# Kernel optimization log

Measured on AMD Instinct MI355X. Metric: run time of the kernel, lower is better.

## Reference

```python
import jax, jax.numpy as jnp
import numpy as np

J = 21        # joints per skeleton
DIM = 3       # cfg.dataset.dim
NH = 7        # node_hsize = 2*DIM + 1
H = 4         # cfg.model.gat_heads
HD = 64       # h_dim
ALPHA = 0.2   # cfg.model.gat_alpha (LeakyReLU slope)


def setup_inputs() -> dict:
    key = jax.random.key(0)
    k1, k2, k3, k4, k5 = jax.random.split(key, 5)
    inputs = jax.random.normal(k1, (16, 1024, J * NH), dtype=jnp.float32)
    starts = jnp.arange(8, dtype=jnp.int64) * 128
    seq_start_end = jnp.stack([starts, starts + 128], axis=1)  # [8,2], unused in forward
    # Xavier-ish scaled params
    W_heads = jax.random.normal(k2, (H, NH, HD), dtype=jnp.float32) * (1.414 / np.sqrt(NH + HD) * np.sqrt(6) / 1.732)
    a_heads = jax.random.normal(k3, (H, 2 * HD), dtype=jnp.float32) * 0.1
    W_out = jax.random.normal(k4, (H * HD, HD), dtype=jnp.float32) * 0.08
    a_out = jax.random.normal(k5, (2 * HD,), dtype=jnp.float32) * 0.1
    return {"inputs": inputs, "seq_start_end": seq_start_end,
            "W_heads": W_heads, "a_heads": a_heads,
            "W_out": W_out, "a_out": a_out}


def _gat_attend(h, a1, a2):
    # h: [..., J, D]; a1,a2: [..., D] broadcastable; FC graph -> no adj mask
    f1 = jnp.sum(h * a1[..., None, :], axis=-1)          # [..., J]
    f2 = jnp.sum(h * a2[..., None, :], axis=-1)          # [..., J]
    e = jax.nn.leaky_relu(f1[..., :, None] + f2[..., None, :], ALPHA)  # [..., J, J]
    attn = jax.nn.softmax(e, axis=-1)
    return jnp.matmul(attn, h)                           # [..., J, D]


def reference(inputs, seq_start_end, W_heads, a_heads, W_out, a_out):
    F_, P, _ = inputs.shape
    # rebuild per-node graph features: [offset(dim) | loc(dim) | S(1)] per joint
    off = inputs[..., : J * DIM].reshape(F_, P, J, DIM)
    loc = inputs[..., J * DIM: 2 * J * DIM].reshape(F_, P, J, DIM)
    S = inputs[..., 2 * J * DIM:].reshape(F_, P, J, 1)
    x = jnp.concatenate([off, loc, S], axis=-1)          # [F,P,J,NH]
    # multi-head GAT layer (concat=True -> elu)
    h = jnp.einsum('fpjn,hnd->fphjd', x, W_heads)        # [F,P,H,J,HD]
    a1 = a_heads[:, :HD]                                 # [H,HD]
    a2 = a_heads[:, HD:]
    hp = jax.nn.elu(_gat_attend(h, a1[None, None], a2[None, None]))  # [F,P,H,J,HD]
    xcat = jnp.transpose(hp, (0, 1, 3, 2, 4)).reshape(F_, P, J, H * HD)
    # output GAT layer (concat=False -> raw h_prime), then outer elu + log_softmax
    h2 = jnp.einsum('fpjn,nd->fpjd', xcat, W_out)        # [F,P,J,HD]
    hp2 = _gat_attend(h2, a_out[None, None, :HD], a_out[None, None, HD:])
    out = jax.nn.log_softmax(jax.nn.elu(hp2), axis=-1)   # log_softmax over feature dim
    return out.reshape(F_, P, J * HD)
```

## Files before the change

kernel.cpp:

```cpp
#include <hip/hip_runtime.h>
#include <hip/hip_bf16.h>
#include <math.h>

#define J   21
#define NH  7
#define H   4
#define HD  64
#define ALPHA 0.2f

#define HPS  264
#define JPA  40
#define JPT  24
#define F12S 24
#define ROW2 68

#define LDS_FLOATS 6612

typedef __attribute__((ext_vector_type(8))) short short8;
typedef __attribute__((ext_vector_type(4))) float floatx4;

static __device__ __forceinline__ short f2bf(float f) {
    __hip_bfloat16 h = __float2bfloat16(f);
    return __builtin_bit_cast(short, h);
}
static __device__ __forceinline__ short hi16(float f) {
    return (short)(__builtin_bit_cast(unsigned, f) >> 16);
}
static __device__ __forceinline__ unsigned pack2hi(float lo, float hi) {
    return __builtin_amdgcn_perm(__builtin_bit_cast(unsigned, hi),
                                 __builtin_bit_cast(unsigned, lo), 0x07060302u);
}
static __device__ __forceinline__ float elu(float a) {
    return (a > 0.f) ? a : (__expf(a) - 1.f);
}

__global__ void preconv(const float* __restrict__ Wo, const float* __restrict__ Wh,
                        const float* __restrict__ ah, short* __restrict__ ws) {
    int t = blockIdx.x * 256 + threadIdx.x;
    if (t < 16384) {
        int n = t >> 8, k = t & 255;
        ws[t] = f2bf(Wo[k * HD + n]);
    } else if (t < 18432) {
        int i = t - 16384;
        int hh = i >> 9, d = (i >> 3) & 63, n = i & 7;
        ws[t] = (n < 7) ? f2bf(Wh[(hh * NH + n) * HD + d]) : (short)0;
    } else if (t < 18496) {
        int i = t - 18432;
        int hh = i >> 4, s = (i >> 3) & 1, n = i & 7;
        float acc = 0.f;
        if (n < 7) {
            for (int d = 0; d < HD; d++)
                acc += Wh[(hh * NH + n) * HD + d] * ah[hh * 2 * HD + s * HD + d];
        }
        ((float*)(ws + 18432))[i] = acc;
    }
}

__global__ __launch_bounds__(256, 6)
void gat_kernel(const float* __restrict__ inp,
                const float* __restrict__ ao,
                const short* __restrict__ ws,
                float* __restrict__ out)
{
    __shared__ __align__(16) float smem[LDS_FLOATS];
    short* hp_bf  = (short*)smem;
    float* f1o    = smem;
    float* f2o    = smem + 24;
    float* f1     = smem + 3344;
    float* f2     = smem + 3440;
    short* h_t    = (short*)(smem + 3536);
    float* h2     = smem + 3536;
    short* h2_t   = (short*)(smem + 4964);

    const short* WoT  = ws;
    const short* WhT  = ws + 16384;
    const float* whaF = (const float*)(ws + 18432);

    const int t    = threadIdx.x;
    const int w    = t >> 6;
    const int lane = t & 63;
    const int quad = lane >> 4;
    const int col  = lane & 15;
    const int rc   = (16 + col < 21) ? (16 + col) : 21;

    const size_t pair = blockIdx.x;
    const float* ip = inp + pair * (size_t)(J * NH);

    for (int e = t; e < 440; e += 256) smem[2904 + e] = 0.f;
    if (t < 4) smem[6608 + t] = 0.f;
    __syncthreads();
    if (t < J * NH) {
        float v = ip[t];
        int j, k;
        if (t < 63)       { j = t / 3;        k = t % 3; }
        else if (t < 126) { j = (t - 63) / 3; k = 3 + (t - 63) % 3; }
        else              { j = t - 126;      k = 6; }
        ((short*)(smem + 2904))[j * JPA + k] = hi16(v);
        smem[t] = v;
    }
    __syncthreads();

    {
        const short* x_bf = (const short*)(smem + 2904);
        short8 xa0 = *(const short8*)(x_bf + col * JPA + quad * 8);
        short8 xa1 = *(const short8*)(x_bf + rc  * JPA + quad * 8);
        #pragma unroll
        for (int nt = 0; nt < 4; nt++) {
            short8 b = *(const short8*)(WhT + ((w * 64 + nt * 16 + col) << 3) + quad * 8);
            floatx4 z = {0.f, 0.f, 0.f, 0.f};
            floatx4 c0 = __builtin_amdgcn_mfma_f32_16x16x32_bf16(xa0, b, z, 0, 0, 0);
            floatx4 c1 = __builtin_amdgcn_mfma_f32_16x16x32_bf16(xa1, b, z, 0, 0, 0);
            short* colbase = h_t + (w * 64 + nt * 16 + col) * JPT;
            #pragma unroll
            for (int r = 0; r < 4; r++) {
                colbase[quad * 4 + r] = hi16(c0[r]);
                int row1 = 16 + quad * 4 + r;
                if (row1 < J) colbase[row1] = hi16(c1[r]);
                else if (row1 < JPT) colbase[row1] = 0;
            }
        }
        if (t < 84) {
            int hh = t / 21, j = t - hh * 21;
            const float* xr = smem;
            float x0 = xr[j*3+0], x1 = xr[j*3+1], x2 = xr[j*3+2];
            float x3 = xr[63+j*3+0], x4 = xr[63+j*3+1], x5 = xr[63+j*3+2];
            float x6 = xr[126+j];
            const float* wp = whaF + hh * 16;
            f1[hh * F12S + j] = x0*wp[0] + x1*wp[1] + x2*wp[2] + x3*wp[3]
                              + x4*wp[4] + x5*wp[5] + x6*wp[6];
            f2[hh * F12S + j] = x0*wp[8] + x1*wp[9] + x2*wp[10] + x3*wp[11]
                              + x4*wp[12] + x5*wp[13] + x6*wp[14];
        }
    }
    __syncthreads();

    {
        float4 fqa = *(const float4*)(f2 + w * F12S + quad * 8);
        float4 fqb = *(const float4*)(f2 + w * F12S + quad * 8 + 4);
        float fq[8] = {fqa.x, fqa.y, fqa.z, fqa.w, fqb.x, fqb.y, fqb.z, fqb.w};
        float fi0 = f1[w * F12S + col];
        const int am  = 16 + col;
        const int amc = (am < 21) ? am : 20;
        float fi1 = f1[w * F12S + amc];
        float e0[8], e1[8];
        float s0 = 0.f, s1 = 0.f;
        #pragma unroll
        for (int j = 0; j < 8; j++) {
            bool valid = (quad * 8 + j) < 21;
            float a0 = fi0 + fq[j]; a0 = (a0 >= 0.f) ? a0 : ALPHA * a0;
            float a1 = fi1 + fq[j]; a1 = (a1 >= 0.f) ? a1 : ALPHA * a1;
            float x0 = __expf(a0); x0 = valid ? x0 : 0.f;
            float x1 = __expf(a1); x1 = valid ? x1 : 0.f;
            e0[j] = x0; e1[j] = x1; s0 += x0; s1 += x1;
        }
        s0 += __shfl_xor(s0, 16); s0 += __shfl_xor(s0, 32);
        s1 += __shfl_xor(s1, 16); s1 += __shfl_xor(s1, 32);
        float inv0 = 1.f / s0, inv1 = 1.f / s1;
        short8 aa0, aa1;
        #pragma unroll
        for (int j = 0; j < 8; j++) {
            aa0[j] = hi16(e0[j] * inv0);
            aa1[j] = hi16(e1[j] * inv1);
        }

        #pragma unroll
        for (int nt = 0; nt < 4; nt++) {
            short8 b = *(const short8*)(h_t + (w * 64 + nt * 16 + col) * JPT + quad * 8);
            floatx4 z = {0.f, 0.f, 0.f, 0.f};
            floatx4 c0 = __builtin_amdgcn_mfma_f32_16x16x32_bf16(aa0, b, z, 0, 0, 0);
            floatx4 c1 = __builtin_amdgcn_mfma_f32_16x16x32_bf16(aa1, b, z, 0, 0, 0);
            #pragma unroll
            for (int r = 0; r < 4; r++) {
                int row0 = quad * 4 + r;
                hp_bf[row0 * HPS + w * 64 + nt * 16 + col] = hi16(elu(c0[r]));
                int row1 = 16 + quad * 4 + r;
                if (row1 < J)
                    hp_bf[row1 * HPS + w * 64 + nt * 16 + col] = hi16(elu(c1[r]));
                else if (row1 == 21)
                    hp_bf[21 * HPS + w * 64 + nt * 16 + col] = 0;
            }
        }
    }
    __syncthreads();

    {
        floatx4 d0 = {0,0,0,0}, d1 = {0,0,0,0};
        #pragma unroll
        for (int s = 0; s < 8; s++) {
            short8 a0 = *(const short8*)(hp_bf + col * HPS + s * 32 + quad * 8);
            short8 a1 = *(const short8*)(hp_bf + rc  * HPS + s * 32 + quad * 8);
            short8 b  = *(const short8*)(WoT + (w * 16 + col) * 256 + s * 32 + quad * 8);
            d0 = __builtin_amdgcn_mfma_f32_16x16x32_bf16(a0, b, d0, 0, 0, 0);
            d1 = __builtin_amdgcn_mfma_f32_16x16x32_bf16(a1, b, d1, 0, 0, 0);
        }
        const int c = w * 16 + col;
        #pragma unroll
        for (int r = 0; r < 4; r++) {
            h2[(quad * 4 + r) * ROW2 + c] = d0[r];
            int row1 = 16 + quad * 4 + r;
            if (row1 < J) h2[row1 * ROW2 + c] = d1[r];
        }
        short* cb = h2_t + c * JPT;
        *(uint2*)(cb + quad * 4) = make_uint2(pack2hi(d0[0], d0[1]), pack2hi(d0[2], d0[3]));
        if (quad == 0)
            *(uint2*)(cb + 16) = make_uint2(pack2hi(d1[0], d1[1]), pack2hi(d1[2], d1[3]));
        else if (quad == 1)
            *(uint2*)(cb + 20) = make_uint2(pack2hi(d1[0], 0.f), 0u);
    }
    __syncthreads();

    if (t < 2 * J) {
        int which = t / J, j = t % J;
        const float4* hrow = (const float4*)(h2 + j * ROW2);
        const float4* ap   = (const float4*)(ao + which * HD);
        float sacc = 0.f;
        #pragma unroll
        for (int k = 0; k < HD / 4; k++) {
            float4 hv = hrow[k], av = ap[k];
            sacc += hv.x*av.x + hv.y*av.y + hv.z*av.z + hv.w*av.w;
        }
        if (which == 0) f1o[j] = sacc; else f2o[j] = sacc;
    }
    __syncthreads();

    {
        const int mt = w & 1;
        const int rh = w >> 1;
        const int arow = mt * 16 + col;
        const int ar = (arow < 21) ? arow : 20;

        float4 fqa = *(const float4*)(f2o + quad * 8);
        float4 fqb = *(const float4*)(f2o + quad * 8 + 4);
        float fq[8] = {fqa.x, fqa.y, fqa.z, fqa.w, fqb.x, fqb.y, fqb.z, fqb.w};
        float fi = f1o[ar];
        float ev[8];
        float ssum = 0.f;
        #pragma unroll
        for (int j = 0; j < 8; j++) {
            bool valid = (quad * 8 + j) < 21;
            float e = fi + fq[j]; e = (e >= 0.f) ? e : ALPHA * e;
            float x = __expf(e); x = valid ? x : 0.f;
            ev[j] = x; ssum += x;
        }
        ssum += __shfl_xor(ssum, 16); ssum += __shfl_xor(ssum, 32);
        float inv = 1.f / ssum;
        short8 a;
        #pragma unroll
        for (int j = 0; j < 8; j++) a[j] = hi16(ev[j] * inv);

        floatx4 acc[4];
        #pragma unroll
        for (int nt = 0; nt < 4; nt++) {
            short8 b = *(const short8*)(h2_t + (nt * 16 + col) * JPT + quad * 8);
            floatx4 z = {0,0,0,0};
            acc[nt] = __builtin_amdgcn_mfma_f32_16x16x32_bf16(a, b, z, 0, 0, 0);
        }
        float* outp = out + pair * (size_t)(J * HD);
        #pragma unroll
        for (int rr = 0; rr < 2; rr++) {
            int r = rh * 2 + rr;
            int row = mt * 16 + quad * 4 + r;
            float v0 = elu(acc[0][r]), v1 = elu(acc[1][r]);
            float v2 = elu(acc[2][r]), v3 = elu(acc[3][r]);
            float s = __expf(v0) + __expf(v1) + __expf(v2) + __expf(v3);
            s += __shfl_xor(s, 1);
            s += __shfl_xor(s, 2);
            s += __shfl_xor(s, 4);
            s += __shfl_xor(s, 8);
            float ls = __logf(s);
            if (row < J) {
                outp[row * HD +      col] = v0 - ls;
                outp[row * HD + 16 + col] = v1 - ls;
                outp[row * HD + 32 + col] = v2 - ls;
                outp[row * HD + 48 + col] = v3 - ls;
            }
        }
    }
}

extern "C" void kernel_launch(void* const* d_in, const int* in_sizes, int n_in,
                              void* d_out, int out_size, void* d_ws, size_t ws_size,
                              hipStream_t stream) {
    const float* inp = (const float*)d_in[0];
    const float* Wh  = (const float*)d_in[2];
    const float* ah  = (const float*)d_in[3];
    const float* Wo  = (const float*)d_in[4];
    const float* ao  = (const float*)d_in[5];
    float* outp = (float*)d_out;
    short* ws   = (short*)d_ws;

    hipLaunchKernelGGL(preconv, dim3(73), dim3(256), 0, stream, Wo, Wh, ah, ws);

    const int pairs = in_sizes[0] / (J * NH);
    hipLaunchKernelGGL(gat_kernel, dim3(pairs), dim3(256), 0, stream,
                       inp, ao, (const short*)ws, outp);
}
```

Before: 219.3 us.

## Fold log2e into logits, vectorize LDS stores, transpose attention MFMA, split dot products

Measured after the change: 201.4 us. 8.1% less time.

```diff
diff --git a/kernel.cpp b/kernel.cpp
--- a/kernel.cpp
+++ b/kernel.cpp
@@ -7,6 +7,7 @@
 #define H   4
 #define HD  64
 #define ALPHA 0.2f
+#define LOG2E 1.44269504f
 
 #define HPS  264
 #define JPA  40
@@ -33,6 +34,17 @@
 static __device__ __forceinline__ float elu(float a) {
     return (a > 0.f) ? a : (__expf(a) - 1.f);
 }
+
+#if __has_builtin(__builtin_amdgcn_exp2f)
+static __device__ __forceinline__ float exp2_fast(float x) { return __builtin_amdgcn_exp2f(x); }
+#else
+static __device__ __forceinline__ float exp2_fast(float x) { return exp2f(x); }
+#endif
+#if __has_builtin(__builtin_amdgcn_rcpf)
+static __device__ __forceinline__ float rcp_fast(float x) { return __builtin_amdgcn_rcpf(x); }
+#else
+static __device__ __forceinline__ float rcp_fast(float x) { return 1.f / x; }
+#endif
 
 __global__ void preconv(const float* __restrict__ Wo, const float* __restrict__ Wh,
                         const float* __restrict__ ah, short* __restrict__ ws) {
@@ -52,7 +64,7 @@
             for (int d = 0; d < HD; d++)
                 acc += Wh[(hh * NH + n) * HD + d] * ah[hh * 2 * HD + s * HD + d];
         }
-        ((float*)(ws + 18432))[i] = acc;
+        ((float*)(ws + 18432))[i] = acc * LOG2E;
     }
 }
 
@@ -111,13 +123,13 @@
             floatx4 c0 = __builtin_amdgcn_mfma_f32_16x16x32_bf16(xa0, b, z, 0, 0, 0);
             floatx4 c1 = __builtin_amdgcn_mfma_f32_16x16x32_bf16(xa1, b, z, 0, 0, 0);
             short* colbase = h_t + (w * 64 + nt * 16 + col) * JPT;
-            #pragma unroll
-            for (int r = 0; r < 4; r++) {
-                colbase[quad * 4 + r] = hi16(c0[r]);
-                int row1 = 16 + quad * 4 + r;
-                if (row1 < J) colbase[row1] = hi16(c1[r]);
-                else if (row1 < JPT) colbase[row1] = 0;
-            }
+            *(uint2*)(colbase + quad * 4) =
+                make_uint2(pack2hi(c0[0], c0[1]), pack2hi(c0[2], c0[3]));
+            if (quad == 0)
+                *(uint2*)(colbase + 16) =
+                    make_uint2(pack2hi(c1[0], c1[1]), pack2hi(c1[2], c1[3]));
+            else if (quad == 1)
+                *(uint2*)(colbase + 20) = make_uint2(pack2hi(c1[0], 0.f), 0u);
         }
         if (t < 84) {
             int hh = t / 21, j = t - hh * 21;
@@ -147,15 +159,15 @@
         #pragma unroll
         for (int j = 0; j < 8; j++) {
             bool valid = (quad * 8 + j) < 21;
-            float a0 = fi0 + fq[j]; a0 = (a0 >= 0.f) ? a0 : ALPHA * a0;
-            float a1 = fi1 + fq[j]; a1 = (a1 >= 0.f) ? a1 : ALPHA * a1;
-            float x0 = __expf(a0); x0 = valid ? x0 : 0.f;
-            float x1 = __expf(a1); x1 = valid ? x1 : 0.f;
+            float a0 = fi0 + fq[j]; a0 = fmaxf(a0, ALPHA * a0);
+            float a1 = fi1 + fq[j]; a1 = fmaxf(a1, ALPHA * a1);
+            float x0 = exp2_fast(a0); x0 = valid ? x0 : 0.f;
+            float x1 = exp2_fast(a1); x1 = valid ? x1 : 0.f;
             e0[j] = x0; e1[j] = x1; s0 += x0; s1 += x1;
         }
         s0 += __shfl_xor(s0, 16); s0 += __shfl_xor(s0, 32);
         s1 += __shfl_xor(s1, 16); s1 += __shfl_xor(s1, 32);
-        float inv0 = 1.f / s0, inv1 = 1.f / s1;
+        float inv0 = rcp_fast(s0), inv1 = rcp_fast(s1);
         short8 aa0, aa1;
         #pragma unroll
         for (int j = 0; j < 8; j++) {
@@ -164,20 +176,21 @@
         }
 
         #pragma unroll
-        for (int nt = 0; nt < 4; nt++) {
-            short8 b = *(const short8*)(h_t + (w * 64 + nt * 16 + col) * JPT + quad * 8);
+        for (int mt = 0; mt < 4; mt++) {
+            short8 a = *(const short8*)(h_t + (w * 64 + mt * 16 + col) * JPT + quad * 8);
             floatx4 z = {0.f, 0.f, 0.f, 0.f};
-            floatx4 c0 = __builtin_amdgcn_mfma_f32_16x16x32_bf16(aa0, b, z, 0, 0, 0);
-            floatx4 c1 = __builtin_amdgcn_mfma_f32_16x16x32_bf16(aa1, b, z, 0, 0, 0);
-            #pragma unroll
-            for (int r = 0; r < 4; r++) {
-                int row0 = quad * 4 + r;
-                hp_bf[row0 * HPS + w * 64 + nt * 16 + col] = hi16(elu(c0[r]));
-                int row1 = 16 + quad * 4 + r;
-                if (row1 < J)
-                    hp_bf[row1 * HPS + w * 64 + nt * 16 + col] = hi16(elu(c1[r]));
-                else if (row1 == 21)
-                    hp_bf[21 * HPS + w * 64 + nt * 16 + col] = 0;
+            floatx4 c0 = __builtin_amdgcn_mfma_f32_16x16x32_bf16(a, aa0, z, 0, 0, 0);
+            floatx4 c1 = __builtin_amdgcn_mfma_f32_16x16x32_bf16(a, aa1, z, 0, 0, 0);
+            short* dst0 = hp_bf + col * HPS + w * 64 + mt * 16 + quad * 4;
+            *(uint2*)dst0 = make_uint2(pack2hi(elu(c0[0]), elu(c0[1])),
+                                       pack2hi(elu(c0[2]), elu(c0[3])));
+            if (am < 21) {
+                short* dst1 = hp_bf + am * HPS + w * 64 + mt * 16 + quad * 4;
+                *(uint2*)dst1 = make_uint2(pack2hi(elu(c1[0]), elu(c1[1])),
+                                           pack2hi(elu(c1[2]), elu(c1[3])));
+            } else if (am == 21) {
+                *(uint2*)(hp_bf + 21 * HPS + w * 64 + mt * 16 + quad * 4) =
+                    make_uint2(0u, 0u);
             }
         }
     }
@@ -209,17 +222,24 @@
     }
     __syncthreads();
 
-    if (t < 2 * J) {
-        int which = t / J, j = t % J;
-        const float4* hrow = (const float4*)(h2 + j * ROW2);
-        const float4* ap   = (const float4*)(ao + which * HD);
+    if (t < 4 * 2 * J) {
+        int which = (t >= 4 * J) ? 1 : 0;
+        int r2 = t - which * 4 * J;
+        int j = r2 >> 2, seg = r2 & 3;
+        const float4* hrow = (const float4*)(h2 + j * ROW2) + seg * 4;
+        const float4* ap   = (const float4*)(ao + which * HD) + seg * 4;
         float sacc = 0.f;
         #pragma unroll
-        for (int k = 0; k < HD / 4; k++) {
+        for (int k = 0; k < 4; k++) {
             float4 hv = hrow[k], av = ap[k];
             sacc += hv.x*av.x + hv.y*av.y + hv.z*av.z + hv.w*av.w;
         }
-        if (which == 0) f1o[j] = sacc; else f2o[j] = sacc;
+        sacc += __shfl_xor(sacc, 1);
+        sacc += __shfl_xor(sacc, 2);
+        if (seg == 0) {
+            float v = sacc * LOG2E;
+            if (which == 0) f1o[j] = v; else f2o[j] = v;
+        }
     }
     __syncthreads();
 
@@ -238,12 +258,12 @@
         #pragma unroll
         for (int j = 0; j < 8; j++) {
             bool valid = (quad * 8 + j) < 21;
-            float e = fi + fq[j]; e = (e >= 0.f) ? e : ALPHA * e;
-            float x = __expf(e); x = valid ? x : 0.f;
+            float e = fi + fq[j]; e = fmaxf(e, ALPHA * e);
+            float x = exp2_fast(e); x = valid ? x : 0.f;
             ev[j] = x; ssum += x;
         }
         ssum += __shfl_xor(ssum, 16); ssum += __shfl_xor(ssum, 32);
-        float inv = 1.f / ssum;
+        float inv = rcp_fast(ssum);
         short8 a;
         #pragma unroll
         for (int j = 0; j < 8; j++) a[j] = hi16(ev[j] * inv);
```
